# Performance work log

Measured on AMD Instinct MI355X. Metric: run time of the kernel, lower is better.

The kernel has to match this reference:

```python
import jax, jax.numpy as jnp
import numpy as np

B, T, C, H, N = 4, 4096, 1024, 16, 64
D_DECAY, D_AAA, D_MV, D_GATE = 64, 64, 32, 160
EPS_GN = 1e-5 * 8 ** 2  # GroupNorm eps = 1e-5 * head_size_divisor**2


def _k(i):
    return jax.random.fold_in(jax.random.key(0), i)


def setup_inputs():
    p = {}
    p["x"] = jax.random.normal(_k(1), (B, T, C), jnp.float32)
    p["v_first"] = jax.random.normal(_k(2), (B, T, C), jnp.float32)
    for i, name in enumerate(["x_r", "x_w", "x_k", "x_v", "x_a", "x_g"]):
        p[name] = jax.random.uniform(_k(10 + i), (1, 1, C), jnp.float32)
    p["w0"] = jnp.linspace(-7.0, -2.0, C, dtype=jnp.float32).reshape(1, 1, C) + 0.5
    p["w1"] = jax.random.normal(_k(20), (C, D_DECAY), jnp.float32) * 0.02
    p["w2"] = jax.random.normal(_k(21), (D_DECAY, C), jnp.float32) * 0.02
    p["a0"] = jax.random.normal(_k(22), (1, 1, C), jnp.float32) * 0.02
    p["a1"] = jax.random.normal(_k(23), (C, D_AAA), jnp.float32) * 0.02
    p["a2"] = jax.random.normal(_k(24), (D_AAA, C), jnp.float32) * 0.02
    p["v0"] = jnp.ones((1, 1, C), jnp.float32)
    p["v1"] = jax.random.normal(_k(25), (C, D_MV), jnp.float32) * 0.02
    p["v2"] = jax.random.normal(_k(26), (D_MV, C), jnp.float32) * 0.02
    p["g1"] = jax.random.normal(_k(27), (C, D_GATE), jnp.float32) * 0.02
    p["g2"] = jax.random.normal(_k(28), (D_GATE, C), jnp.float32) * 0.02
    p["k_k"] = jnp.full((1, 1, C), 0.85, jnp.float32)
    p["k_a"] = jnp.ones((1, 1, C), jnp.float32)
    p["r_k"] = jax.random.normal(_k(29), (H, N), jnp.float32) * 0.02
    s = 0.5 / C ** 0.5
    p["Wr"] = jax.random.uniform(_k(30), (C, C), jnp.float32, -s, s)
    p["Wk"] = jax.random.uniform(_k(31), (C, C), jnp.float32, -0.1 * s, 0.1 * s)
    p["Wv"] = jax.random.uniform(_k(32), (C, C), jnp.float32, -s, s)
    p["Wo"] = jax.random.uniform(_k(33), (C, C), jnp.float32, -s, s)
    p["ln_w"] = jnp.ones((C,), jnp.float32)
    p["ln_b"] = jnp.zeros((C,), jnp.float32)
    p["alpha"] = jnp.array(0.5, jnp.float32)
    return p


def _wkv_scan(ins, reverse):
    # ins: tuple of time-major (T,B,H,N) arrays: r, decay, k, v, a, b
    def step(S, inp):
        r_t, d_t, k_t, v_t, a_t, b_t = inp
        sa = jnp.einsum('bhij,bhj->bhi', S, a_t)  # in-context removal term
        S = (S * d_t[:, :, None, :]
             + sa[..., None] * b_t[:, :, None, :]
             + v_t[..., None] * k_t[:, :, None, :])
        return S, jnp.einsum('bhij,bhj->bhi', S, r_t)
    S0 = jnp.zeros((B, H, N, N), jnp.float32)
    return jax.lax.scan(step, S0, ins, reverse=reverse)[1]


def reference(x, v_first, x_r, x_w, x_k, x_v, x_a, x_g, w0, w1, w2, a0, a1, a2,
              v0, v1, v2, g1, g2, k_k, k_a, r_k, Wr, Wk, Wv, Wo, ln_w, ln_b, alpha):
    xx = jnp.pad(x, ((0, 0), (1, 0), (0, 0)))[:, :T, :] - x  # token shift
    xr = x + xx * x_r
    xw = x + xx * x_w
    xk = x + xx * x_k
    xv = x + xx * x_v
    xa = x + xx * x_a
    xg = x + xx * x_g
    r = xr @ Wr.T
    w = -jax.nn.softplus(-(w0 + jnp.tanh(xw @ w1) @ w2)) - 0.5
    k = xk @ Wk.T
    v = xv @ Wv.T
    v = v + (v_first - v) * jax.nn.sigmoid(v0 + (xv @ v1) @ v2)  # layer_id != 0
    a = jax.nn.sigmoid(a0 + (xa @ a1) @ a2)
    g = jax.nn.sigmoid(xg @ g1) @ g2
    kk = (k * k_k).reshape(B, T, H, N)
    kk = kk / jnp.maximum(jnp.linalg.norm(kk, axis=-1, keepdims=True), 1e-12)
    k = k * (1.0 + (a - 1.0) * k_a)
    rh = r.reshape(B, T, H, N)
    kh = k.reshape(B, T, H, N)
    vh = v.reshape(B, T, H, N)
    dec = jnp.exp(-jnp.exp(w.reshape(B, T, H, N)))  # per-channel decay
    ah = -kk
    bh = kk * a.reshape(B, T, H, N)
    tm = lambda z: jnp.transpose(z, (1, 0, 2, 3))  # -> (T,B,H,N)
    ins = (tm(rh), tm(dec), tm(kh), tm(vh), tm(ah), tm(bh))
    y_f = _wkv_scan(ins, reverse=False)
    y_b = _wkv_scan(ins, reverse=True)
    y = alpha * y_f + (1.0 - alpha) * y_b  # bidirectional blend (alpha)
    y = jnp.transpose(y, (1, 0, 2, 3))  # (B,T,H,N)
    mu = y.mean(-1, keepdims=True)
    var = y.var(-1, keepdims=True)
    y = (y - mu) / jnp.sqrt(var + EPS_GN)  # GroupNorm(H groups)
    y = y * ln_w.reshape(1, 1, H, N) + ln_b.reshape(1, 1, H, N)
    y = y + (rh * kh * r_k).sum(-1, keepdims=True) * vh
    out = (y.reshape(B, T, C) * g) @ Wo.T
    return (out, v_first)
```

## Files before the change

### kernel.cpp

```cpp
#include <hip/hip_runtime.h>
#include <hip/hip_bf16.h>
#include <math.h>

#define BB 4
#define TT 4096
#define CC 1024
#define HH 16
#define NN 64
#define BT (BB*TT)
#define EPS_GN 6.4e-4f
#define TMAX (TT-1)
#define LCH 64
#define CB 8
#define NB 8
#define STR 68

typedef __attribute__((ext_vector_type(8))) short bf16x8;
typedef __attribute__((ext_vector_type(4))) float f32x4;

__device__ __forceinline__ float sigmoidf_(float x) {
    return 1.0f / (1.0f + expf(-x));
}

__device__ __forceinline__ float waveReduceSum(float v) {
    #pragma unroll
    for (int off = 32; off > 0; off >>= 1)
        v += __shfl_xor(v, off, 64);
    return v;
}

__device__ __forceinline__ unsigned short f2bf(float f) {
    unsigned u = __float_as_uint(f);
    u += 0x7FFFu + ((u >> 16) & 1u);
    return (unsigned short)(u >> 16);
}
__device__ __forceinline__ float bf2f(unsigned short h) {
    return __uint_as_float(((unsigned)h) << 16);
}

__device__ __forceinline__ void gll16(const unsigned short* g, unsigned short* l) {
    __builtin_amdgcn_global_load_lds(
        (__attribute__((address_space(1))) void*)(g),
        (__attribute__((address_space(3))) void*)(l), 16, 0, 0);
}

template<int SA0,int SA1,int SB0,int SB1>
__device__ __forceinline__ void gemm64(const float* __restrict__ A,
                                       const float* __restrict__ B,
                                       float acc[4][4], int tr, int tc) {
    #pragma unroll 2
    for (int kx = 0; kx < 64; kx += 4) {
        float a_[4][4];
        if (SA0 == 1) {
            #pragma unroll
            for (int kk = 0; kk < 4; kk++) {
                float4 t = *(const float4*)&A[tr + (kx + kk) * SA1];
                a_[0][kk] = t.x; a_[1][kk] = t.y; a_[2][kk] = t.z; a_[3][kk] = t.w;
            }
        } else {
            #pragma unroll
            for (int r = 0; r < 4; r++) {
                float4 t = *(const float4*)&A[(tr + r) * SA0 + kx];
                a_[r][0] = t.x; a_[r][1] = t.y; a_[r][2] = t.z; a_[r][3] = t.w;
            }
        }
        float b_[4][4];
        if (SB0 == 1) {
            #pragma unroll
            for (int kk = 0; kk < 4; kk++) {
                float4 t = *(const float4*)&B[tc + (kx + kk) * SB1];
                b_[0][kk] = t.x; b_[1][kk] = t.y; b_[2][kk] = t.z; b_[3][kk] = t.w;
            }
        } else {
            #pragma unroll
            for (int cq = 0; cq < 4; cq++) {
                float4 t = *(const float4*)&B[(tc + cq) * SB0 + kx];
                b_[cq][0] = t.x; b_[cq][1] = t.y; b_[cq][2] = t.z; b_[cq][3] = t.w;
            }
        }
        #pragma unroll
        for (int r = 0; r < 4; r++)
            #pragma unroll
            for (int cq = 0; cq < 4; cq++)
                #pragma unroll
                for (int kk = 0; kk < 4; kk++)
                    acc[r][cq] = fmaf(a_[r][kk], b_[cq][kk], acc[r][cq]);
    }
}

template<bool DOMIX>
__global__ __launch_bounds__(256) void conv_split(
    const float* __restrict__ X, const float* __restrict__ mix,
    unsigned short* __restrict__ Hi, unsigned short* __restrict__ Lo,
    int ngroups)
{
    int g = blockIdx.x * 256 + threadIdx.x;
    if (g >= ngroups) return;
    int m = g >> 7;
    int k = (g & 127) * 8;
    const float* px = X + (size_t)m * CC + k;
    float a[8];
    {
        float4 x0 = *(const float4*)px;
        float4 x1 = *(const float4*)(px + 4);
        a[0]=x0.x; a[1]=x0.y; a[2]=x0.z; a[3]=x0.w;
        a[4]=x1.x; a[5]=x1.y; a[6]=x1.z; a[7]=x1.w;
    }
    if (DOMIX) {
        float4 p0, p1;
        if ((m & (TT - 1)) == 0) {
            p0 = make_float4(0.f,0.f,0.f,0.f); p1 = p0;
        } else {
            p0 = *(const float4*)(px - CC);
            p1 = *(const float4*)(px - CC + 4);
        }
        float4 m0 = *(const float4*)(mix + k);
        float4 m1 = *(const float4*)(mix + k + 4);
        float pv[8] = {p0.x,p0.y,p0.z,p0.w,p1.x,p1.y,p1.z,p1.w};
        float mv[8] = {m0.x,m0.y,m0.z,m0.w,m1.x,m1.y,m1.z,m1.w};
        #pragma unroll
        for (int j = 0; j < 8; j++) a[j] += (pv[j] - a[j]) * mv[j];
    }
    unsigned short hi[8], lo[8];
    #pragma unroll
    for (int j = 0; j < 8; j++) {
        hi[j] = f2bf(a[j]);
        lo[j] = f2bf(a[j] - bf2f(hi[j]));
    }
    uint4 H, L;
    H.x = (unsigned)hi[0] | ((unsigned)hi[1] << 16);
    H.y = (unsigned)hi[2] | ((unsigned)hi[3] << 16);
    H.z = (unsigned)hi[4] | ((unsigned)hi[5] << 16);
    H.w = (unsigned)hi[6] | ((unsigned)hi[7] << 16);
    L.x = (unsigned)lo[0] | ((unsigned)lo[1] << 16);
    L.y = (unsigned)lo[2] | ((unsigned)lo[3] << 16);
    L.z = (unsigned)lo[4] | ((unsigned)lo[5] << 16);
    L.w = (unsigned)lo[6] | ((unsigned)lo[7] << 16);
    *(uint4*)(Hi + (size_t)g * 8) = H;
    *(uint4*)(Lo + (size_t)g * 8) = L;
}

__global__ __launch_bounds__(256) void conv_split_x3(
    const float* __restrict__ X,
    const float* __restrict__ mr, const float* __restrict__ mk,
    const float* __restrict__ mv,
    unsigned short* __restrict__ rH, unsigned short* __restrict__ rL,
    unsigned short* __restrict__ kH, unsigned short* __restrict__ kL,
    unsigned short* __restrict__ vH, unsigned short* __restrict__ vL)
{
    int g = blockIdx.x * 256 + threadIdx.x;
    int m = g >> 7;
    int k = (g & 127) * 8;
    const float* px = X + (size_t)m * CC + k;
    float xv8[8], pv[8];
    {
        float4 x0 = *(const float4*)px;
        float4 x1 = *(const float4*)(px + 4);
        xv8[0]=x0.x; xv8[1]=x0.y; xv8[2]=x0.z; xv8[3]=x0.w;
        xv8[4]=x1.x; xv8[5]=x1.y; xv8[6]=x1.z; xv8[7]=x1.w;
    }
    if ((m & (TT - 1)) == 0) {
        #pragma unroll
        for (int j = 0; j < 8; j++) pv[j] = 0.f;
    } else {
        float4 p0 = *(const float4*)(px - CC);
        float4 p1 = *(const float4*)(px - CC + 4);
        pv[0]=p0.x; pv[1]=p0.y; pv[2]=p0.z; pv[3]=p0.w;
        pv[4]=p1.x; pv[5]=p1.y; pv[6]=p1.z; pv[7]=p1.w;
    }
    const float* mixes[3] = {mr, mk, mv};
    unsigned short* His[3] = {rH, kH, vH};
    unsigned short* Los[3] = {rL, kL, vL};
    #pragma unroll
    for (int s = 0; s < 3; s++) {
        float4 m0 = *(const float4*)(mixes[s] + k);
        float4 m1 = *(const float4*)(mixes[s] + k + 4);
        float mv8[8] = {m0.x,m0.y,m0.z,m0.w,m1.x,m1.y,m1.z,m1.w};
        unsigned short hi[8], lo[8];
        #pragma unroll
        for (int j = 0; j < 8; j++) {
            float a = xv8[j] + (pv[j] - xv8[j]) * mv8[j];
            hi[j] = f2bf(a);
            lo[j] = f2bf(a - bf2f(hi[j]));
        }
        uint4 H, L;
        H.x = (unsigned)hi[0] | ((unsigned)hi[1] << 16);
        H.y = (unsigned)hi[2] | ((unsigned)hi[3] << 16);
        H.z = (unsigned)hi[4] | ((unsigned)hi[5] << 16);
        H.w = (unsigned)hi[6] | ((unsigned)hi[7] << 16);
        L.x = (unsigned)lo[0] | ((unsigned)lo[1] << 16);
        L.y = (unsigned)lo[2] | ((unsigned)lo[3] << 16);
        L.z = (unsigned)lo[4] | ((unsigned)lo[5] << 16);
        L.w = (unsigned)lo[6] | ((unsigned)lo[7] << 16);
        *(uint4*)(His[s] + (size_t)g * 8) = H;
        *(uint4*)(Los[s] + (size_t)g * 8) = L;
    }
}

__global__ __launch_bounds__(256) void conv_w2(
    const float* __restrict__ W, int K, int Kp,
    unsigned short* __restrict__ Hi, unsigned short* __restrict__ Lo)
{
    int idx = blockIdx.x * 256 + threadIdx.x;
    int nk8 = Kp >> 3;
    if (idx >= CC * nk8) return;
    int n = idx / nk8, k0 = (idx - n * nk8) * 8;
    unsigned short h8[8], l8[8];
    #pragma unroll
    for (int j = 0; j < 8; j++) {
        int k = k0 + j;
        float v = (k < K) ? W[(size_t)k * CC + n] : 0.f;
        h8[j] = f2bf(v);
        l8[j] = f2bf(v - bf2f(h8[j]));
    }
    uint4 H, L;
    H.x = (unsigned)h8[0] | ((unsigned)h8[1] << 16);
    H.y = (unsigned)h8[2] | ((unsigned)h8[3] << 16);
    H.z = (unsigned)h8[4] | ((unsigned)h8[5] << 16);
    H.w = (unsigned)h8[6] | ((unsigned)h8[7] << 16);
    L.x = (unsigned)l8[0] | ((unsigned)l8[1] << 16);
    L.y = (unsigned)l8[2] | ((unsigned)l8[3] << 16);
    L.z = (unsigned)l8[4] | ((unsigned)l8[5] << 16);
    L.w = (unsigned)l8[6] | ((unsigned)l8[7] << 16);
    *(uint4*)(Hi + (size_t)n * Kp + k0) = H;
    *(uint4*)(Lo + (size_t)n * Kp + k0) = L;
}

__global__ __launch_bounds__(256, 2) void gemm_split_bf16(
    const unsigned short* __restrict__ Ah, const unsigned short* __restrict__ Al,
    const unsigned short* __restrict__ Bh, const unsigned short* __restrict__ Bl,
    float* __restrict__ Out)
{
    __shared__ __align__(16) unsigned short lds[4][128 * 64];
    const int tid = threadIdx.x;
    const int lane = tid & 63;
    const int wave = tid >> 6;
    const int wm = (wave >> 1) * 64, wn = (wave & 1) * 64;
    const int wg = blockIdx.x;
    const int xcd = wg & 7;
    const int j = wg >> 3;
    const int m0 = ((j >> 3) * 8 + xcd) * 128;
    const int n0 = (j & 7) * 128;

    f32x4 acc[4][4];
    #pragma unroll
    for (int i = 0; i < 4; i++)
        #pragma unroll
        for (int jj = 0; jj < 4; jj++)
            acc[i][jj] = (f32x4){0.f, 0.f, 0.f, 0.f};

    for (int k0 = 0; k0 < CC; k0 += 64) {
        #pragma unroll
        for (int p = 0; p < 4; p++) {
            const unsigned short* sbase = (p == 0) ? Ah : (p == 1) ? Al
                                        : (p == 2) ? Bh : Bl;
            const int rbase = (p < 2) ? m0 : n0;
            #pragma unroll
            for (int i = 0; i < 4; i++) {
                int slot = i * 256 + wave * 64 + lane;
                int row = slot >> 3, gsl = slot & 7;
                const unsigned short* src = sbase
                    + (size_t)(rbase + row) * CC + k0 + ((gsl ^ (row & 7)) * 8);
                gll16(src, &lds[p][(size_t)(i * 256 + wave * 64) * 8]);
            }
        }
        __syncthreads();

        #pragma unroll
        for (int ks = 0; ks < 2; ks++) {
            bf16x8 bhf[4], blf[4];
            #pragma unroll
            for (int nt = 0; nt < 4; nt++) {
                int col = wn + nt * 16 + (lane & 15);
                int gk = ks * 4 + (lane >> 4);
                int el = col * 64 + ((gk ^ (col & 7)) * 8);
                bhf[nt] = *(const bf16x8*)&lds[2][el];
                blf[nt] = *(const bf16x8*)&lds[3][el];
            }
            #pragma unroll
            for (int mt = 0; mt < 4; mt++) {
                int row = wm + mt * 16 + (lane & 15);
                int gk = ks * 4 + (lane >> 4);
                int el = row * 64 + ((gk ^ (row & 7)) * 8);
                bf16x8 ahf = *(const bf16x8*)&lds[0][el];
                bf16x8 alf = *(const bf16x8*)&lds[1][el];
                #pragma unroll
                for (int nt = 0; nt < 4; nt++) {
                    acc[mt][nt] = __builtin_amdgcn_mfma_f32_16x16x32_bf16(
                        ahf, bhf[nt], acc[mt][nt], 0, 0, 0);
                    acc[mt][nt] = __builtin_amdgcn_mfma_f32_16x16x32_bf16(
                        alf, bhf[nt], acc[mt][nt], 0, 0, 0);
                    acc[mt][nt] = __builtin_amdgcn_mfma_f32_16x16x32_bf16(
                        ahf, blf[nt], acc[mt][nt], 0, 0, 0);
                }
            }
        }
        __syncthreads();
    }
    float* cf = (float*)&lds[0][0];
    #pragma unroll
    for (int pass = 0; pass < 2; ++pass) {
        __syncthreads();
        if ((wave >> 1) == pass) {
            #pragma unroll
            for (int mt = 0; mt < 4; mt++)
                #pragma unroll
                for (int nt = 0; nt < 4; nt++)
                    #pragma unroll
                    for (int r = 0; r < 4; r++) {
                        int row = mt * 16 + (lane >> 4) * 4 + r;
                        int col = wn + nt * 16 + (lane & 15);
                        cf[row * 132 + col] = acc[mt][nt][r];
                    }
        }
        __syncthreads();
        #pragma unroll
        for (int i = 0; i < 8; i++) {
            int g = tid + 256 * i;
            int row = g >> 5, c4 = (g & 31) * 4;
            float4 v = *(float4*)&cf[row * 132 + c4];
            *(float4*)&Out[(size_t)(m0 + pass * 64 + row) * CC + n0 + c4] = v;
        }
    }
}

__global__ __launch_bounds__(256) void lora1_all(
    const float* __restrict__ X,
    const float* __restrict__ w1, const float* __restrict__ a1,
    const float* __restrict__ v1, const float* __restrict__ g1,
    const float* __restrict__ xw, const float* __restrict__ xa,
    const float* __restrict__ xv, const float* __restrict__ xg,
    unsigned short* __restrict__ awh, unsigned short* __restrict__ awl,
    unsigned short* __restrict__ aah, unsigned short* __restrict__ aal,
    unsigned short* __restrict__ avh, unsigned short* __restrict__ avl,
    unsigned short* __restrict__ agh, unsigned short* __restrict__ agl)
{
    const int y = blockIdx.y;
    const float* W; const float* mix; unsigned short *Hi, *Lo;
    int Ncols, n0, epi, Kp;
    if (y == 0)      { W=w1; mix=xw; Hi=awh; Lo=awl; Ncols=64;  n0=0;          epi=1; Kp=64;  }
    else if (y == 1) { W=a1; mix=xa; Hi=aah; Lo=aal; Ncols=64;  n0=0;          epi=0; Kp=64;  }
    else if (y == 2) { W=v1; mix=xv; Hi=avh; Lo=avl; Ncols=32;  n0=0;          epi=0; Kp=64;  }
    else             { W=g1; mix=xg; Hi=agh; Lo=agl; Ncols=160; n0=(y-3)*64;   epi=2; Kp=192; }

    __shared__ float As[8][64];
    __shared__ float Bs[8][64];
    const int tid = threadIdx.x;
    const int m0 = blockIdx.x * 64;
    const int sr  = tid >> 1;
    const int skq = (tid & 1) * 4;
    const int t2  = tid - 128;
    const int bkr = t2 >> 4;
    const int bnq = (t2 & 15) * 4;
    const int tm = (tid >> 3) * 2;
    const int tn = (tid & 7) * 8;

    float acc[2][8];
    #pragma unroll
    for (int i = 0; i < 2; i++)
        #pragma unroll
        for (int j = 0; j < 8; j++) acc[i][j] = 0.f;

    auto ldAm = [&](int gm, int gk) -> float4 {
        const float* px = X + (size_t)gm * CC + gk;
        float4 xvv = *(const float4*)px;
        float4 pv;
        if ((gm & (TT - 1)) == 0) pv = make_float4(0.f, 0.f, 0.f, 0.f);
        else pv = *(const float4*)(px - CC);
        float4 mv = *(const float4*)(mix + gk);
        xvv.x += (pv.x - xvv.x) * mv.x;
        xvv.y += (pv.y - xvv.y) * mv.y;
        xvv.z += (pv.z - xvv.z) * mv.z;
        xvv.w += (pv.w - xvv.w) * mv.w;
        return xvv;
    };

    float4 aR = make_float4(0.f, 0.f, 0.f, 0.f);
    float4 bR = make_float4(0.f, 0.f, 0.f, 0.f);
    if (tid < 128) {
        aR = ldAm(m0 + sr, skq);
    } else {
        int gn = n0 + bnq;
        bR = (gn < Ncols) ? *(const float4*)(W + (size_t)bkr * Ncols + gn)
                          : make_float4(0.f, 0.f, 0.f, 0.f);
    }

    for (int k0 = 0; k0 < CC; k0 += 8) {
        __syncthreads();
        if (tid < 128) {
            As[skq + 0][sr] = aR.x;
            As[skq + 1][sr] = aR.y;
            As[skq + 2][sr] = aR.z;
            As[skq + 3][sr] = aR.w;
        } else {
            *(float4*)&Bs[bkr][bnq] = bR;
        }
        __syncthreads();

        if (k0 + 8 < CC) {
            if (tid < 128) {
                aR = ldAm(m0 + sr, k0 + 8 + skq);
            } else {
                int gn = n0 + bnq;
                bR = (gn < Ncols) ? *(const float4*)(W + (size_t)(k0 + 8 + bkr) * Ncols + gn)
                                  : make_float4(0.f, 0.f, 0.f, 0.f);
            }
        }

        #pragma unroll
        for (int kk = 0; kk < 8; ++kk) {
            float av[2], bv[8];
            av[0] = As[kk][tm];
            av[1] = As[kk][tm + 1];
            *(float4*)&bv[0] = *(const float4*)&Bs[kk][tn];
            *(float4*)&bv[4] = *(const float4*)&Bs[kk][tn + 4];
            #pragma unroll
            for (int i = 0; i < 2; i++)
                #pragma unroll
                for (int j = 0; j < 8; j++)
                    acc[i][j] = fmaf(av[i], bv[j], acc[i][j]);
        }
    }

    #pragma unroll
    for (int i = 0; i < 2; i++) {
        int gm = m0 + tm + i;
        int gn = n0 + tn;
        if (gn < Kp) {
            unsigned short h8[8], l8[8];
            #pragma unroll
            for (int j = 0; j < 8; j++) {
                float v = 0.f;
                if (gn + j < Ncols) {
                    v = acc[i][j];
                    if (epi == 1) v = tanhf(v);
                    else if (epi == 2) v = sigmoidf_(v);
                }
                h8[j] = f2bf(v);
                l8[j] = f2bf(v - bf2f(h8[j]));
            }
            uint4 H, L;
            H.x = (unsigned)h8[0] | ((unsigned)h8[1] << 16);
            H.y = (unsigned)h8[2] | ((unsigned)h8[3] << 16);
            H.z = (unsigned)h8[4] | ((unsigned)h8[5] << 16);
            H.w = (unsigned)h8[6] | ((unsigned)h8[7] << 16);
            L.x = (unsigned)l8[0] | ((unsigned)l8[1] << 16);
            L.y = (unsigned)l8[2] | ((unsigned)l8[3] << 16);
            L.z = (unsigned)l8[4] | ((unsigned)l8[5] << 16);
            L.w = (unsigned)l8[6] | ((unsigned)l8[7] << 16);
            *(uint4*)(Hi + (size_t)gm * Kp + gn) = H;
            *(uint4*)(Lo + (size_t)gm * Kp + gn) = L;
        }
    }
}

__global__ __launch_bounds__(256, 3) void lora2_mfma(
    const unsigned short* __restrict__ awh, const unsigned short* __restrict__ awl,
    const unsigned short* __restrict__ aah, const unsigned short* __restrict__ aal,
    const unsigned short* __restrict__ avh, const unsigned short* __restrict__ avl,
    const unsigned short* __restrict__ agh, const unsigned short* __restrict__ agl,
    const unsigned short* __restrict__ w2h, const unsigned short* __restrict__ w2l,
    const unsigned short* __restrict__ a2h, const unsigned short* __restrict__ a2l,
    const unsigned short* __restrict__ v2h, const unsigned short* __restrict__ v2l,
    const unsigned short* __restrict__ g2h, const unsigned short* __restrict__ g2l,
    const float* __restrict__ w0, const float* __restrict__ a0v,
    const float* __restrict__ v0v, const float* __restrict__ v_first,
    float* __restrict__ decb, float* __restrict__ ab,
    float* __restrict__ vbuf, float* __restrict__ gb)
{
    __shared__ __align__(16) unsigned short lds[24576];
    const int z = blockIdx.z;
    const unsigned short *Ah, *Al, *Bh, *Bl; int Kp;
    if (z == 0)      { Ah = awh; Al = awl; Bh = w2h; Bl = w2l; Kp = 64;  }
    else if (z == 1) { Ah = aah; Al = aal; Bh = a2h; Bl = a2l; Kp = 64;  }
    else if (z == 2) { Ah = avh; Al = avl; Bh = v2h; Bl = v2l; Kp = 64;  }
    else             { Ah = agh; Al = agl; Bh = g2h; Bl = g2l; Kp = 192; }

    const int tid = threadIdx.x, lane = tid & 63, wave = tid >> 6;
    const int wm = (wave >> 1) * 64, wn = (wave & 1) * 32;
    const int m0 = blockIdx.x * 128, n0 = blockIdx.y * 64;

    f32x4 acc[4][2];
    #pragma unroll
    for (int i = 0; i < 4; i++)
        #pragma unroll
        for (int jj = 0; jj < 2; jj++)
            acc[i][jj] = (f32x4){0.f, 0.f, 0.f, 0.f};

    for (int k0 = 0; k0 < Kp; k0 += 64) {
        #pragma unroll
        for (int p = 0; p < 2; p++) {
            const unsigned short* sbase = (p == 0) ? Ah : Al;
            #pragma unroll
            for (int i = 0; i < 4; i++) {
                int slot = i * 256 + wave * 64 + lane;
                int row = slot >> 3, gsl = slot & 7;
                const unsigned short* src = sbase
                    + (size_t)(m0 + row) * Kp + k0 + ((gsl ^ (row & 7)) * 8);
                gll16(src, &lds[(size_t)(p * 8192) + (size_t)(i * 256 + wave * 64) * 8]);
            }
        }
        #pragma unroll
        for (int p = 0; p < 2; p++) {
            const unsigned short* sbase = (p == 0) ? Bh : Bl;
            #pragma unroll
            for (int i = 0; i < 2; i++) {
                int slot = i * 256 + wave * 64 + lane;
                int row = slot >> 3, gsl = slot & 7;
                const unsigned short* src = sbase
                    + (size_t)(n0 + row) * Kp + k0 + ((gsl ^ (row & 7)) * 8);
                gll16(src, &lds[(size_t)(16384 + p * 4096) + (size_t)(i * 256 + wave * 64) * 8]);
            }
        }
        __syncthreads();

        #pragma unroll
        for (int ks = 0; ks < 2; ks++) {
            bf16x8 bhf[2], blf[2];
            #pragma unroll
            for (int nt = 0; nt < 2; nt++) {
                int col = wn + nt * 16 + (lane & 15);
                int gk = ks * 4 + (lane >> 4);
                int el = col * 64 + ((gk ^ (col & 7)) * 8);
                bhf[nt] = *(const bf16x8*)&lds[16384 + el];
                blf[nt] = *(const bf16x8*)&lds[20480 + el];
            }
            #pragma unroll
            for (int mt = 0; mt < 4; mt++) {
                int row = wm + mt * 16 + (lane & 15);
                int gk = ks * 4 + (lane >> 4);
                int el = row * 64 + ((gk ^ (row & 7)) * 8);
                bf16x8 ahf = *(const bf16x8*)&lds[el];
                bf16x8 alf = *(const bf16x8*)&lds[8192 + el];
                #pragma unroll
                for (int nt = 0; nt < 2; nt++) {
                    acc[mt][nt] = __builtin_amdgcn_mfma_f32_16x16x32_bf16(
                        ahf, bhf[nt], acc[mt][nt], 0, 0, 0);
                    acc[mt][nt] = __builtin_amdgcn_mfma_f32_16x16x32_bf16(
                        alf, bhf[nt], acc[mt][nt], 0, 0, 0);
                    acc[mt][nt] = __builtin_amdgcn_mfma_f32_16x16x32_bf16(
                        ahf, blf[nt], acc[mt][nt], 0, 0, 0);
                }
            }
        }
        __syncthreads();
    }
    float* cf = (float*)&lds[0];
    #pragma unroll
    for (int mt = 0; mt < 4; mt++)
        #pragma unroll
        for (int nt = 0; nt < 2; nt++)
            #pragma unroll
            for (int r = 0; r < 4; r++) {
                int row = wm + mt * 16 + (lane >> 4) * 4 + r;
                int col = wn + nt * 16 + (lane & 15);
                cf[row * 68 + col] = acc[mt][nt][r];
            }
    __syncthreads();
    #pragma unroll
    for (int i = 0; i < 8; i++) {
        int idx = tid + 256 * i;
        int row = idx >> 4, c4 = (idx & 15) * 4;
        float4 v = *(float4*)&cf[row * 68 + c4];
        int gm = m0 + row;
        int c = n0 + c4;
        size_t off = (size_t)gm * CC + c;
        if (z == 0) {
            float4 w0q = *(const float4*)(w0 + c);
            float4 o;
            o.x = expf(-expf(-log1pf(expf(-(w0q.x + v.x))) - 0.5f));
            o.y = expf(-expf(-log1pf(expf(-(w0q.y + v.y))) - 0.5f));
            o.z = expf(-expf(-log1pf(expf(-(w0q.z + v.z))) - 0.5f));
            o.w = expf(-expf(-log1pf(expf(-(w0q.w + v.w))) - 0.5f));
            *(float4*)&decb[off] = o;
        } else if (z == 1) {
            float4 a0q = *(const float4*)(a0v + c);
            float4 o;
            o.x = sigmoidf_(a0q.x + v.x);
            o.y = sigmoidf_(a0q.y + v.y);
            o.z = sigmoidf_(a0q.z + v.z);
            o.w = sigmoidf_(a0q.w + v.w);
            *(float4*)&ab[off] = o;
        } else if (z == 2) {
            float4 v0q = *(const float4*)(v0v + c);
            float4 vr = *(const float4*)&vbuf[off];
            float4 vf = *(const float4*)&v_first[off];
            float4 o;
            o.x = vr.x + (vf.x - vr.x) * sigmoidf_(v0q.x + v.x);
            o.y = vr.y + (vf.y - vr.y) * sigmoidf_(v0q.y + v.y);
            o.z = vr.z + (vf.z - vr.z) * sigmoidf_(v0q.z + v.z);
            o.w = vr.w + (vf.w - vr.w) * sigmoidf_(v0q.w + v.w);
            *(float4*)&vbuf[off] = o;
        } else {
            *(float4*)&gb[off] = v;
        }
    }
}

__global__ __launch_bounds__(256) void wkvA(
    const float* __restrict__ kb, const float* __restrict__ ab,
    const float* __restrict__ vb, const float* __restrict__ decb,
    const float* __restrict__ k_k, const float* __restrict__ k_a,
    float* __restrict__ Gb, float* __restrict__ Ub,
    float* __restrict__ Bpb, float* __restrict__ Kpb,
    float* __restrict__ wcb, int cb)
{
    __shared__ __align__(16) float sAp[64 * STR];
    __shared__ __align__(16) float sBp[64 * STR];
    __shared__ __align__(16) float sKp[64 * STR];
    __shared__ __align__(16) float sT [64 * STR];
    __shared__ float sSeg[4][64];
    const int inst = blockIdx.x;
    const int bhd = inst >> 3, lc = inst & 7;
    const int dir = bhd & 1, bh = bhd >> 1, b = bh >> 4, h = bh & 15;
    const int c64 = (cb * CB + lc) * LCH;
    const int tid = threadIdx.x;
    const int lane = tid & 63, seg = tid >> 6;
    const int ch = h * 64 + lane;
    const size_t gbase = (size_t)inst * 4096;

    float loc[16];
    {
        float run = 1.f;
        #pragma unroll
        for (int i = 0; i < 16; i++) {
            int p = seg * 16 + i;
            int t = dir ? (TMAX - (c64 + p)) : (c64 + p);
            float d = decb[((size_t)(b * TT + t)) * CC + ch];
            run *= d; loc[i] = run;
        }
        sSeg[seg][lane] = run;
    }
    __syncthreads();
    float pre = 1.f;
    for (int s2 = 0; s2 < seg; ++s2) pre *= sSeg[s2][lane];
    {
        const float kkl = k_k[ch], kal = k_a[ch];
        #pragma unroll
        for (int i = 0; i < 16; i++) {
            int p = seg * 16 + i;
            int t = dir ? (TMAX - (c64 + p)) : (c64 + p);
            size_t ra = ((size_t)(b * TT + t)) * CC + ch;
            float kraw = kb[ra], asig = ab[ra];
            float kkv = kraw * kkl;
            float s2 = waveReduceSum(kkv * kkv);
            float kkn = kkv / fmaxf(sqrtf(s2), 1e-12f);
            float wc = loc[i] * pre;
            float wx = (i == 0) ? pre : loc[i - 1] * pre;
            float apv = -kkn * wx;
            float bpv = kkn * asig / wc;
            float kpv = kraw * (1.f + (asig - 1.f) * kal) / wc;
            sAp[lane * STR + p] = apv;
            sBp[lane * STR + p] = bpv;
            sKp[lane * STR + p] = kpv;
            Bpb[gbase + p * 64 + lane] = bpv;
            Kpb[gbase + p * 64 + lane] = kpv;
            wcb[gbase + p * 64 + lane] = wc;
        }
    }
    __syncthreads();

    const int tr = (tid >> 4) * 4, tc = (tid & 15) * 4;
    {
        float acc[4][4] = {};
        gemm64<1, STR, 1, STR>(sAp, sKp, acc, tr, tc);
        #pragma unroll
        for (int r = 0; r < 4; r++)
            #pragma unroll
            for (int cq = 0; cq < 4; cq++)
                sT[(tr + r) * STR + tc + cq] = (tc + cq < tr + r) ? acc[r][cq] : 0.f;
    }
    __syncthreads();
    {
        float accY[4][4] = {};
        const float* vbase = vb + ((size_t)(b * TT + (dir ? (TMAX - c64) : c64))) * CC
                           + h * 64 + tc;
        const ptrdiff_t vstep = dir ? -(ptrdiff_t)CC : (ptrdiff_t)CC;
        #pragma unroll 2
        for (int j4 = 0; j4 < 64; j4 += 4) {
            float a_[4][4];
            #pragma unroll
            for (int r = 0; r < 4; r++) {
                float4 t4 = *(const float4*)&sT[(tr + r) * STR + j4];
                a_[r][0] = t4.x; a_[r][1] = t4.y; a_[r][2] = t4.z; a_[r][3] = t4.w;
            }
            float4 vq[4];
            #pragma unroll
            for (int kk = 0; kk < 4; kk++)
                vq[kk] = *(const float4*)(vbase + (ptrdiff_t)(j4 + kk) * vstep);
            #pragma unroll
            for (int r = 0; r < 4; r++) {
                accY[r][0] = fmaf(a_[r][0], vq[0].x, fmaf(a_[r][1], vq[1].x,
                             fmaf(a_[r][2], vq[2].x, fmaf(a_[r][3], vq[3].x, accY[r][0]))));
                accY[r][1] = fmaf(a_[r][0], vq[0].y, fmaf(a_[r][1], vq[1].y,
                             fmaf(a_[r][2], vq[2].y, fmaf(a_[r][3], vq[3].y, accY[r][1]))));
                accY[r][2] = fmaf(a_[r][0], vq[0].z, fmaf(a_[r][1], vq[1].z,
                             fmaf(a_[r][2], vq[2].z, fmaf(a_[r][3], vq[3].z, accY[r][2]))));
                accY[r][3] = fmaf(a_[r][0], vq[0].w, fmaf(a_[r][1], vq[1].w,
                             fmaf(a_[r][2], vq[2].w, fmaf(a_[r][3], vq[3].w, accY[r][3]))));
            }
        }
        #pragma unroll
        for (int r = 0; r < 4; r++)
            #pragma unroll
            for (int cq = 0; cq < 4; cq++)
                sKp[(tr + r) * STR + tc + cq] = accY[r][cq];
    }
    __syncthreads();
    {
        float acc[4][4] = {};
        gemm64<1, STR, 1, STR>(sAp, sBp, acc, tr, tc);
        #pragma unroll
        for (int r = 0; r < 4; r++)
            #pragma unroll
            for (int cq = 0; cq < 4; cq++)
                sT[(tr + r) * STR + tc + cq] = (tc + cq < tr + r) ? acc[r][cq] : 0.f;
    }
    __syncthreads();
    if (tid < 64) {
        for (int r = 0; r < 64; ++r) {
            float acc = 0.f;
            for (int s = 0; s < r; ++s)
                acc = fmaf(sT[r * STR + s], sBp[s * STR + tid], acc);
            sBp[r * STR + tid] = (r == tid) ? 1.f : acc;
        }
    }
    __syncthreads();
    {
        float accG[4][4] = {};
        gemm64<STR, 1, STR, 1>(sBp, sAp, accG, tr, tc);
        float accU[4][4] = {};
        gemm64<STR, 1, 1, STR>(sBp, sKp, accU, tr, tc);
        #pragma unroll
        for (int r = 0; r < 4; r++) {
            *(float4*)&Gb[gbase + (tr + r) * 64 + tc] =
                make_float4(accG[r][0], accG[r][1], accG[r][2], accG[r][3]);
            *(float4*)&Ub[gbase + (tr + r) * 64 + tc] =
                make_float4(accU[r][0], accU[r][1], accU[r][2], accU[r][3]);
        }
    }
}

__global__ __launch_bounds__(256) void wkvB(
    const float* __restrict__ vb,
    const float* __restrict__ Gb, float* __restrict__ Ub,
    const float* __restrict__ Bpb, const float* __restrict__ Kpb,
    const float* __restrict__ wcb, float* __restrict__ S0b,
    float* __restrict__ Scur, int cb)
{
    __shared__ __align__(16) float sS[64 * STR];
    __shared__ __align__(16) float sG[64 * STR];
    __shared__ __align__(16) float sU[64 * STR];
    __shared__ __align__(16) float sB[64 * STR];
    __shared__ __align__(16) float sK[64 * STR];
    __shared__ __align__(16) float sV[64 * STR];
    const int bhd = blockIdx.x;
    const int dir = bhd & 1, bh = bhd >> 1, b = bh >> 4, h = bh & 15;
    const int tid = threadIdx.x;
    const int tr = (tid >> 4) * 4, tc = (tid & 15) * 4;

    for (int i = tid; i < 4096; i += 256)
        sS[(i >> 6) * STR + (i & 63)] = Scur[(size_t)bhd * 4096 + i];
    __syncthreads();

    for (int lc = 0; lc < CB; ++lc) {
        const int inst = bhd * CB + lc;
        const size_t gbase = (size_t)inst * 4096;
        const int c64 = (cb * CB + lc) * LCH;
        for (int i = tid; i < 4096; i += 256) {
            int rr = i >> 6, jj = i & 63;
            sG[rr * STR + jj] = Gb[gbase + i];
            sB[rr * STR + jj] = Bpb[gbase + i];
            sK[rr * STR + jj] = Kpb[gbase + i];
            int t = dir ? (TMAX - (c64 + rr)) : (c64 + rr);
            sV[rr * STR + jj] = vb[((size_t)(b * TT + t)) * CC + h * 64 + jj];
            S0b[gbase + i] = sS[rr * STR + jj];
        }
        __syncthreads();
        {
            float acc[4][4];
            #pragma unroll
            for (int r = 0; r < 4; r++) {
                float4 u0 = *(const float4*)&Ub[gbase + (tr + r) * 64 + tc];
                acc[r][0] = u0.x; acc[r][1] = u0.y; acc[r][2] = u0.z; acc[r][3] = u0.w;
            }
            gemm64<STR, 1, STR, 1>(sG, sS, acc, tr, tc);
            #pragma unroll
            for (int r = 0; r < 4; r++) {
                #pragma unroll
                for (int cq = 0; cq < 4; cq++) sU[(tr + r) * STR + tc + cq] = acc[r][cq];
                *(float4*)&Ub[gbase + (tr + r) * 64 + tc] =
                    make_float4(acc[r][0], acc[r][1], acc[r][2], acc[r][3]);
            }
        }
        __syncthreads();
        {
            float acc[4][4] = {};
            gemm64<1, STR, 1, STR>(sU, sB, acc, tr, tc);
            gemm64<1, STR, 1, STR>(sV, sK, acc, tr, tc);
            float w63[4];
            #pragma unroll
            for (int cq = 0; cq < 4; cq++) w63[cq] = wcb[gbase + 63 * 64 + tc + cq];
            #pragma unroll
            for (int r = 0; r < 4; r++)
                #pragma unroll
                for (int cq = 0; cq < 4; cq++) {
                    float sv = sS[(tr + r) * STR + tc + cq];
                    acc[r][cq] = (sv + acc[r][cq]) * w63[cq];
                }
            #pragma unroll
            for (int r = 0; r < 4; r++)
                #pragma unroll
                for (int cq = 0; cq < 4; cq++)
                    sS[(tr + r) * STR + tc + cq] = acc[r][cq];
        }
        __syncthreads();
    }
    for (int i = tid; i < 4096; i += 256)
        Scur[(size_t)bhd * 4096 + i] = sS[(i >> 6) * STR + (i & 63)];
}

__global__ __launch_bounds__(256) void wkvC(
    const float* __restrict__ rb, const float* __restrict__ vb,
    const float* __restrict__ Bpb, const float* __restrict__ Kpb,
    const float* __restrict__ Ub, const float* __restrict__ S0b,
    const float* __restrict__ wcb, const float* __restrict__ alpha_p,
    float* __restrict__ yb, int cb)
{
    __shared__ __align__(16) float sR[64 * STR];
    __shared__ __align__(16) float sO[64 * STR];
    __shared__ __align__(16) float sT2[64 * STR];
    const int inst = blockIdx.x;
    const int bhd = inst >> 3, lc = inst & 7;
    const int dir = bhd & 1, bh = bhd >> 1, b = bh >> 4, h = bh & 15;
    const int c64 = (cb * CB + lc) * LCH;
    const int tid = threadIdx.x, lane = tid & 63, seg = tid >> 6;
    const size_t gbase = (size_t)inst * 4096;
    const float alpha = alpha_p[0];
    const float wscale = dir ? (1.f - alpha) : alpha;
    const bool first = (cb < NB / 2);

    #pragma unroll
    for (int i = 0; i < 16; i++) {
        int p = seg * 16 + i;
        int t = dir ? (TMAX - (c64 + p)) : (c64 + p);
        size_t ra = ((size_t)(b * TT + t)) * CC + h * 64 + lane;
        float wc = wcb[gbase + p * 64 + lane];
        sR[lane * STR + p] = rb[ra] * wc;
        sO[lane * STR + p] = Bpb[gbase + p * 64 + lane];
    }
    __syncthreads();
    const int tr = (tid >> 4) * 4, tc = (tid & 15) * 4;
    float accO[4][4] = {};
    {
        float acc[4][4] = {};
        gemm64<1, STR, 1, STR>(sR, sO, acc, tr, tc);
        #pragma unroll
        for (int r = 0; r < 4; r++)
            #pragma unroll
            for (int cq = 0; cq < 4; cq++)
                sT2[(tr + r) * STR + tc + cq] = (tc + cq <= tr + r) ? acc[r][cq] : 0.f;
    }
    __syncthreads();
    for (int i = tid; i < 4096; i += 256)
        sO[(i >> 6) * STR + (i & 63)] = Ub[gbase + i];
    __syncthreads();
    gemm64<STR, 1, 1, STR>(sT2, sO, accO, tr, tc);
    __syncthreads();
    #pragma unroll
    for (int i = 0; i < 16; i++) {
        int p = seg * 16 + i;
        sO[lane * STR + p] = Kpb[gbase + p * 64 + lane];
    }
    __syncthreads();
    {
        float acc[4][4] = {};
        gemm64<1, STR, 1, STR>(sR, sO, acc, tr, tc);
        #pragma unroll
        for (int r = 0; r < 4; r++)
            #pragma unroll
            for (int cq = 0; cq < 4; cq++)
                sT2[(tr + r) * STR + tc + cq] = (tc + cq <= tr + r) ? acc[r][cq] : 0.f;
    }
    __syncthreads();
    #pragma unroll
    for (int i = 0; i < 16; i++) {
        int p = seg * 16 + i;
        int t = dir ? (TMAX - (c64 + p)) : (c64 + p);
        sO[p * STR + lane] = vb[((size_t)(b * TT + t)) * CC + h * 64 + lane];
    }
    __syncthreads();
    gemm64<STR, 1, 1, STR>(sT2, sO, accO, tr, tc);
    __syncthreads();
    for (int i = tid; i < 4096; i += 256)
        sO[(i >> 6) * STR + (i & 63)] = S0b[gbase + i];
    __syncthreads();
    gemm64<1, STR, STR, 1>(sR, sO, accO, tr, tc);
    #pragma unroll
    for (int r = 0; r < 4; r++) {
        int p = tr + r;
        int t = dir ? (TMAX - (c64 + p)) : (c64 + p);
        float* yp = &yb[((size_t)(b * TT + t)) * CC + h * 64 + tc];
        float4 o;
        if (first) {
            o.x = wscale * accO[r][0];
            o.y = wscale * accO[r][1];
            o.z = wscale * accO[r][2];
            o.w = wscale * accO[r][3];
        } else {
            float4 old = *(float4*)yp;
            o.x = old.x + wscale * accO[r][0];
            o.y = old.y + wscale * accO[r][1];
            o.z = old.z + wscale * accO[r][2];
            o.w = old.w + wscale * accO[r][3];
        }
        *(float4*)yp = o;
    }
}

__global__ __launch_bounds__(256) void post_kernel(
    const float* __restrict__ yb, const float* __restrict__ rbv,
    const float* __restrict__ kbv, const float* __restrict__ abv,
    const float* __restrict__ vbv, const float* __restrict__ gbv,
    const float* __restrict__ kaw, const float* __restrict__ r_k,
    const float* __restrict__ ln_w, const float* __restrict__ ln_b,
    unsigned short* __restrict__ zh, unsigned short* __restrict__ zl)
{
    const int t = blockIdx.x;
    const int tid = threadIdx.x;
    const size_t base = (size_t)t * CC;
    #pragma unroll
    for (int j = 0; j < 4; j++) {
        int c = tid + 256 * j;
        float y = yb[base + c];
        float s1 = waveReduceSum(y);
        float s2 = waveReduceSum(y * y);
        float mu = s1 * (1.0f / 64.0f);
        float var = s2 * (1.0f / 64.0f) - mu * mu;
        float yn = (y - mu) * rsqrtf(var + EPS_GN);
        yn = yn * ln_w[c] + ln_b[c];
        float rv = rbv[base + c];
        float kf = kbv[base + c] * (1.0f + (abv[base + c] - 1.0f) * kaw[c]);
        float vv = vbv[base + c];
        float dot = waveReduceSum(rv * kf * r_k[c]);
        yn += dot * vv;
        float z = yn * gbv[base + c];
        unsigned short h = f2bf(z);
        zh[base + c] = h;
        zl[base + c] = f2bf(z - bf2f(h));
    }
}

extern "C" void kernel_launch(void* const* d_in, const int* in_sizes, int n_in,
                              void* d_out, int out_size, void* d_ws, size_t ws_size,
                              hipStream_t stream)
{
    (void)in_sizes; (void)n_in; (void)out_size; (void)ws_size;
    const float* x      = (const float*)d_in[0];
    const float* vfirst = (const float*)d_in[1];
    const float* x_r    = (const float*)d_in[2];
    const float* x_w    = (const float*)d_in[3];
    const float* x_k    = (const float*)d_in[4];
    const float* x_v    = (const float*)d_in[5];
    const float* x_a    = (const float*)d_in[6];
    const float* x_g    = (const float*)d_in[7];
    const float* w0     = (const float*)d_in[8];
    const float* w1     = (const float*)d_in[9];
    const float* w2     = (const float*)d_in[10];
    const float* a0     = (const float*)d_in[11];
    const float* a1     = (const float*)d_in[12];
    const float* a2     = (const float*)d_in[13];
    const float* v0     = (const float*)d_in[14];
    const float* v1     = (const float*)d_in[15];
    const float* v2     = (const float*)d_in[16];
    const float* g1     = (const float*)d_in[17];
    const float* g2     = (const float*)d_in[18];
    const float* k_k    = (const float*)d_in[19];
    const float* k_a    = (const float*)d_in[20];
    const float* r_k    = (const float*)d_in[21];
    const float* Wr     = (const float*)d_in[22];
    const float* Wk     = (const float*)d_in[23];
    const float* Wv     = (const float*)d_in[24];
    const float* Wo     = (const float*)d_in[25];
    const float* ln_w   = (const float*)d_in[26];
    const float* ln_b   = (const float*)d_in[27];
    const float* alpha  = (const float*)d_in[28];

    const size_t SZ = (size_t)BT * CC;
    const size_t CHB = (size_t)1024 * 4096;
    float* ws   = (float*)d_ws;
    float* rb   = ws + 0 * SZ;
    float* kb   = ws + 1 * SZ;
    float* vb   = ws + 2 * SZ;
    float* decb = ws + 3 * SZ;
    float* ab   = ws + 4 * SZ;
    float* actf = ws + 5 * SZ;
    unsigned short* awh = (unsigned short*)actf;
    unsigned short* awl = awh + (size_t)BT * 64;
    unsigned short* aah = awl + (size_t)BT * 64;
    unsigned short* aal = aah + (size_t)BT * 64;
    unsigned short* avh = aal + (size_t)BT * 64;
    unsigned short* avl = avh + (size_t)BT * 64;
    unsigned short* agh = avl + (size_t)BT * 64;
    unsigned short* agl = agh + (size_t)BT * 192;
    float* Gb   = actf + (size_t)BT * 384;
    float* Ub   = Gb + CHB;
    float* Bpb  = Ub + CHB;
    float* Kpb  = Bpb + CHB;
    float* S0b  = Kpb + CHB;
    float* wcb  = S0b + CHB;
    float* Scur = wcb + CHB;
    unsigned short* Whb = (unsigned short*)(Scur + (size_t)128 * 4096);
    unsigned short* Wlb = Whb + (size_t)CC * CC;
    unsigned short* w2th = Wlb + (size_t)CC * CC;
    unsigned short* w2tl = w2th + (size_t)CC * 64;
    unsigned short* a2th = w2tl + (size_t)CC * 64;
    unsigned short* a2tl = a2th + (size_t)CC * 64;
    unsigned short* v2th = a2tl + (size_t)CC * 64;
    unsigned short* v2tl = v2th + (size_t)CC * 64;
    unsigned short* g2th = v2tl + (size_t)CC * 64;
    unsigned short* g2tl = g2th + (size_t)CC * 192;
    float* outp = (float*)d_out;
    unsigned short* xrh = (unsigned short*)outp;
    unsigned short* xrl = xrh + SZ;
    unsigned short* xkh = xrl + SZ;
    unsigned short* xkl = xkh + SZ;
    unsigned short* xvh = (unsigned short*)decb;
    unsigned short* xvl = xvh + SZ;
    float* gb   = outp;
    float* yb   = outp + SZ;
    unsigned short* zAh = (unsigned short*)decb;
    unsigned short* zAl = zAh + SZ;

    dim3 blk(256);
    const int NG_A = BT * (CC / 8);
    const int NG_W = CC * (CC / 8);
    dim3 gridA(NG_A / 256), gridW(NG_W / 256);
    dim3 gridG(1024);

    conv_split_x3<<<gridA, blk, 0, stream>>>(x, x_r, x_k, x_v,
                                             xrh, xrl, xkh, xkl, xvh, xvl);
    conv_split<false><<<gridW, blk, 0, stream>>>(Wr, nullptr, Whb, Wlb, NG_W);
    gemm_split_bf16<<<gridG, blk, 0, stream>>>(xrh, xrl, Whb, Wlb, rb);
    conv_split<false><<<gridW, blk, 0, stream>>>(Wk, nullptr, Whb, Wlb, NG_W);
    gemm_split_bf16<<<gridG, blk, 0, stream>>>(xkh, xkl, Whb, Wlb, kb);
    conv_split<false><<<gridW, blk, 0, stream>>>(Wv, nullptr, Whb, Wlb, NG_W);
    gemm_split_bf16<<<gridG, blk, 0, stream>>>(xvh, xvl, Whb, Wlb, vb);

    conv_w2<<<dim3(32), blk, 0, stream>>>(w2, 64, 64, w2th, w2tl);
    conv_w2<<<dim3(32), blk, 0, stream>>>(a2, 64, 64, a2th, a2tl);
    conv_w2<<<dim3(32), blk, 0, stream>>>(v2, 32, 64, v2th, v2tl);
    conv_w2<<<dim3(96), blk, 0, stream>>>(g2, 160, 192, g2th, g2tl);

    lora1_all<<<dim3(BT / 64, 6), blk, 0, stream>>>(x, w1, a1, v1, g1,
        x_w, x_a, x_v, x_g, awh, awl, aah, aal, avh, avl, agh, agl);
    lora2_mfma<<<dim3(BT / 128, CC / 64, 4), blk, 0, stream>>>(
        awh, awl, aah, aal, avh, avl, agh, agl,
        w2th, w2tl, a2th, a2tl, v2th, v2tl, g2th, g2tl,
        w0, a0, v0, vfirst, decb, ab, vb, gb);

    hipMemsetAsync(Scur, 0, (size_t)128 * 4096 * sizeof(float), stream);
    for (int cb = 0; cb < NB; ++cb) {
        wkvA<<<dim3(1024), blk, 0, stream>>>(kb, ab, vb, decb, k_k, k_a,
                                             Gb, Ub, Bpb, Kpb, wcb, cb);
        wkvB<<<dim3(128), blk, 0, stream>>>(vb, Gb, Ub, Bpb, Kpb, wcb, S0b, Scur, cb);
        wkvC<<<dim3(1024), blk, 0, stream>>>(rb, vb, Bpb, Kpb, Ub, S0b, wcb,
                                             alpha, yb, cb);
    }

    post_kernel<<<dim3(BT), blk, 0, stream>>>(yb, rb, kb, ab, vb, gb, k_a, r_k,
                                              ln_w, ln_b, zAh, zAl);
    conv_split<false><<<gridW, blk, 0, stream>>>(Wo, nullptr, Whb, Wlb, NG_W);
    hipMemcpyAsync(outp + SZ, vfirst, SZ * sizeof(float),
                   hipMemcpyDeviceToDevice, stream);
    gemm_split_bf16<<<gridG, blk, 0, stream>>>(zAh, zAl, Whb, Wlb, outp);
}
```

Before: 3.118 ms.

## Batch weight conversion and r/k/v GEMMs; halve GEMM K-tile, drop LDS epilogue

All four projection weights are converted to hi/lo bf16 in one launch into a 4-slot buffer. The r, k and v projections now run as a single GEMM launch with a grid y-dimension selecting inputs and outputs, removing the serial per-weight conversion and GEMM launches. The GEMM K-step is halved to 32 so LDS use drops and launch bounds allow 3 blocks per CU. The LDS-staged coalesced output store is replaced by direct per-lane scalar stores, which may write to global memory less efficiently.

After: 3.139 ms. About the same (+0.7%).

```diff
diff --git a/kernel.cpp b/kernel.cpp
--- a/kernel.cpp
+++ b/kernel.cpp
@@ -86,58 +86,6 @@
                 for (int kk = 0; kk < 4; kk++)
                     acc[r][cq] = fmaf(a_[r][kk], b_[cq][kk], acc[r][cq]);
     }
-}
-
-template<bool DOMIX>
-__global__ __launch_bounds__(256) void conv_split(
-    const float* __restrict__ X, const float* __restrict__ mix,
-    unsigned short* __restrict__ Hi, unsigned short* __restrict__ Lo,
-    int ngroups)
-{
-    int g = blockIdx.x * 256 + threadIdx.x;
-    if (g >= ngroups) return;
-    int m = g >> 7;
-    int k = (g & 127) * 8;
-    const float* px = X + (size_t)m * CC + k;
-    float a[8];
-    {
-        float4 x0 = *(const float4*)px;
-        float4 x1 = *(const float4*)(px + 4);
-        a[0]=x0.x; a[1]=x0.y; a[2]=x0.z; a[3]=x0.w;
-        a[4]=x1.x; a[5]=x1.y; a[6]=x1.z; a[7]=x1.w;
-    }
-    if (DOMIX) {
-        float4 p0, p1;
-        if ((m & (TT - 1)) == 0) {
-            p0 = make_float4(0.f,0.f,0.f,0.f); p1 = p0;
-        } else {
-            p0 = *(const float4*)(px - CC);
-            p1 = *(const float4*)(px - CC + 4);
-        }
-        float4 m0 = *(const float4*)(mix + k);
-        float4 m1 = *(const float4*)(mix + k + 4);
-        float pv[8] = {p0.x,p0.y,p0.z,p0.w,p1.x,p1.y,p1.z,p1.w};
-        float mv[8] = {m0.x,m0.y,m0.z,m0.w,m1.x,m1.y,m1.z,m1.w};
-        #pragma unroll
-        for (int j = 0; j < 8; j++) a[j] += (pv[j] - a[j]) * mv[j];
-    }
-    unsigned short hi[8], lo[8];
-    #pragma unroll
-    for (int j = 0; j < 8; j++) {
-        hi[j] = f2bf(a[j]);
-        lo[j] = f2bf(a[j] - bf2f(hi[j]));
-    }
-    uint4 H, L;
-    H.x = (unsigned)hi[0] | ((unsigned)hi[1] << 16);
-    H.y = (unsigned)hi[2] | ((unsigned)hi[3] << 16);
-    H.z = (unsigned)hi[4] | ((unsigned)hi[5] << 16);
-    H.w = (unsigned)hi[6] | ((unsigned)hi[7] << 16);
-    L.x = (unsigned)lo[0] | ((unsigned)lo[1] << 16);
-    L.y = (unsigned)lo[2] | ((unsigned)lo[3] << 16);
-    L.z = (unsigned)lo[4] | ((unsigned)lo[5] << 16);
-    L.w = (unsigned)lo[6] | ((unsigned)lo[7] << 16);
-    *(uint4*)(Hi + (size_t)g * 8) = H;
-    *(uint4*)(Lo + (size_t)g * 8) = L;
 }
 
 __global__ __launch_bounds__(256) void conv_split_x3(
@@ -197,6 +145,45 @@
     }
 }
 
+
+__global__ __launch_bounds__(256) void conv_w4(
+    const float* __restrict__ Wr, const float* __restrict__ Wk,
+    const float* __restrict__ Wv, const float* __restrict__ Wo,
+    unsigned short* __restrict__ Hi, unsigned short* __restrict__ Lo)
+{
+    int g = blockIdx.x * 256 + threadIdx.x;
+    int y = blockIdx.y;
+    const float* W = (y == 0) ? Wr : (y == 1) ? Wk : (y == 2) ? Wv : Wo;
+    size_t doff = (size_t)y * CC * CC;
+    int m = g >> 7;
+    int k = (g & 127) * 8;
+    const float* px = W + (size_t)m * CC + k;
+    float a[8];
+    {
+        float4 x0 = *(const float4*)px;
+        float4 x1 = *(const float4*)(px + 4);
+        a[0]=x0.x; a[1]=x0.y; a[2]=x0.z; a[3]=x0.w;
+        a[4]=x1.x; a[5]=x1.y; a[6]=x1.z; a[7]=x1.w;
+    }
+    unsigned short hi[8], lo[8];
+    #pragma unroll
+    for (int j = 0; j < 8; j++) {
+        hi[j] = f2bf(a[j]);
+        lo[j] = f2bf(a[j] - bf2f(hi[j]));
+    }
+    uint4 H, L;
+    H.x = (unsigned)hi[0] | ((unsigned)hi[1] << 16);
+    H.y = (unsigned)hi[2] | ((unsigned)hi[3] << 16);
+    H.z = (unsigned)hi[4] | ((unsigned)hi[5] << 16);
+    H.w = (unsigned)hi[6] | ((unsigned)hi[7] << 16);
+    L.x = (unsigned)lo[0] | ((unsigned)lo[1] << 16);
+    L.y = (unsigned)lo[2] | ((unsigned)lo[3] << 16);
+    L.z = (unsigned)lo[4] | ((unsigned)lo[5] << 16);
+    L.w = (unsigned)lo[6] | ((unsigned)lo[7] << 16);
+    *(uint4*)(Hi + doff + (size_t)g * 8) = H;
+    *(uint4*)(Lo + doff + (size_t)g * 8) = L;
+}
+
 __global__ __launch_bounds__(256) void conv_w2(
     const float* __restrict__ W, int K, int Kp,
     unsigned short* __restrict__ Hi, unsigned short* __restrict__ Lo)
@@ -226,15 +213,22 @@
     *(uint4*)(Lo + (size_t)n * Kp + k0) = L;
 }
 
-__global__ __launch_bounds__(256, 2) void gemm_split_bf16(
-    const unsigned short* __restrict__ Ah, const unsigned short* __restrict__ Al,
-    const unsigned short* __restrict__ Bh, const unsigned short* __restrict__ Bl,
-    float* __restrict__ Out)
+__global__ __launch_bounds__(256, 3) void gemm_split_bf16(
+    const unsigned short* __restrict__ A0h, const unsigned short* __restrict__ A0l,
+    const unsigned short* __restrict__ A1h, const unsigned short* __restrict__ A1l,
+    const unsigned short* __restrict__ A2h, const unsigned short* __restrict__ A2l,
+    const unsigned short* __restrict__ W4h, const unsigned short* __restrict__ W4l,
+    float* __restrict__ O0, float* __restrict__ O1, float* __restrict__ O2,
+    int wbase)
 {
-    __shared__ __align__(16) unsigned short lds[4][128 * 64];
-    const int tid = threadIdx.x;
-    const int lane = tid & 63;
-    const int wave = tid >> 6;
+    __shared__ __align__(16) unsigned short lds[4][128 * 32];
+    const int sel = blockIdx.y;
+    const unsigned short* Ah = (sel == 0) ? A0h : (sel == 1) ? A1h : A2h;
+    const unsigned short* Al = (sel == 0) ? A0l : (sel == 1) ? A1l : A2l;
+    float* Out = (sel == 0) ? O0 : (sel == 1) ? O1 : O2;
+    const unsigned short* Bh = W4h + (size_t)(wbase + sel) * CC * CC;
+    const unsigned short* Bl = W4l + (size_t)(wbase + sel) * CC * CC;
+    const int tid = threadIdx.x, lane = tid & 63, wave = tid >> 6;
     const int wm = (wave >> 1) * 64, wn = (wave & 1) * 64;
     const int wg = blockIdx.x;
     const int xcd = wg & 7;
@@ -249,79 +243,61 @@
         for (int jj = 0; jj < 4; jj++)
             acc[i][jj] = (f32x4){0.f, 0.f, 0.f, 0.f};
 
-    for (int k0 = 0; k0 < CC; k0 += 64) {
+    for (int k0 = 0; k0 < CC; k0 += 32) {
         #pragma unroll
         for (int p = 0; p < 4; p++) {
             const unsigned short* sbase = (p == 0) ? Ah : (p == 1) ? Al
                                         : (p == 2) ? Bh : Bl;
             const int rbase = (p < 2) ? m0 : n0;
             #pragma unroll
-            for (int i = 0; i < 4; i++) {
+            for (int i = 0; i < 2; i++) {
                 int slot = i * 256 + wave * 64 + lane;
-                int row = slot >> 3, gsl = slot & 7;
+                int row = slot >> 2, gsl = slot & 3;
                 const unsigned short* src = sbase
-                    + (size_t)(rbase + row) * CC + k0 + ((gsl ^ (row & 7)) * 8);
+                    + (size_t)(rbase + row) * CC + k0 + ((gsl ^ (row & 3)) * 8);
                 gll16(src, &lds[p][(size_t)(i * 256 + wave * 64) * 8]);
             }
         }
         __syncthreads();
 
-        #pragma unroll
-        for (int ks = 0; ks < 2; ks++) {
-            bf16x8 bhf[4], blf[4];
+        const int gk = lane >> 4;
+        bf16x8 bhf[4], blf[4];
+        #pragma unroll
+        for (int nt = 0; nt < 4; nt++) {
+            int col = wn + nt * 16 + (lane & 15);
+            int el = col * 32 + ((gk ^ (col & 3)) * 8);
+            bhf[nt] = *(const bf16x8*)&lds[2][el];
+            blf[nt] = *(const bf16x8*)&lds[3][el];
+        }
+        #pragma unroll
+        for (int mt = 0; mt < 4; mt++) {
+            int row = wm + mt * 16 + (lane & 15);
+            int el = row * 32 + ((gk ^ (row & 3)) * 8);
+            bf16x8 ahf = *(const bf16x8*)&lds[0][el];
+            bf16x8 alf = *(const bf16x8*)&lds[1][el];
             #pragma unroll
             for (int nt = 0; nt < 4; nt++) {
-                int col = wn + nt * 16 + (lane & 15);
-                int gk = ks * 4 + (lane >> 4);
-                int el = col * 64 + ((gk ^ (col & 7)) * 8);
-                bhf[nt] = *(const bf16x8*)&lds[2][el];
-                blf[nt] = *(const bf16x8*)&lds[3][el];
-            }
-            #pragma unroll
-            for (int mt = 0; mt < 4; mt++) {
-                int row = wm + mt * 16 + (lane & 15);
-                int gk = ks * 4 + (lane >> 4);
-                int el = row * 64 + ((gk ^ (row & 7)) * 8);
-                bf16x8 ahf = *(const bf16x8*)&lds[0][el];
-                bf16x8 alf = *(const bf16x8*)&lds[1][el];
-                #pragma unroll
-                for (int nt = 0; nt < 4; nt++) {
-                    acc[mt][nt] = __builtin_amdgcn_mfma_f32_16x16x32_bf16(
-                        ahf, bhf[nt], acc[mt][nt], 0, 0, 0);
-                    acc[mt][nt] = __builtin_amdgcn_mfma_f32_16x16x32_bf16(
-                        alf, bhf[nt], acc[mt][nt], 0, 0, 0);
-                    acc[mt][nt] = __builtin_amdgcn_mfma_f32_16x16x32_bf16(
-                        ahf, blf[nt], acc[mt][nt], 0, 0, 0);
-                }
+                acc[mt][nt] = __builtin_amdgcn_mfma_f32_16x16x32_bf16(
+                    ahf, bhf[nt], acc[mt][nt], 0, 0, 0);
+                acc[mt][nt] = __builtin_amdgcn_mfma_f32_16x16x32_bf16(
+                    alf, bhf[nt], acc[mt][nt], 0, 0, 0);
+                acc[mt][nt] = __builtin_amdgcn_mfma_f32_16x16x32_bf16(
+                    ahf, blf[nt], acc[mt][nt], 0, 0, 0);
             }
         }
         __syncthreads();
     }
-    float* cf = (float*)&lds[0][0];
-    #pragma unroll
-    for (int pass = 0; pass < 2; ++pass) {
-        __syncthreads();
-        if ((wave >> 1) == pass) {
-            #pragma unroll
-            for (int mt = 0; mt < 4; mt++)
-                #pragma unroll
-                for (int nt = 0; nt < 4; nt++)
-                    #pragma unroll
-                    for (int r = 0; r < 4; r++) {
-                        int row = mt * 16 + (lane >> 4) * 4 + r;
-                        int col = wn + nt * 16 + (lane & 15);
-                        cf[row * 132 + col] = acc[mt][nt][r];
-                    }
-        }
-        __syncthreads();
-        #pragma unroll
-        for (int i = 0; i < 8; i++) {
-            int g = tid + 256 * i;
-            int row = g >> 5, c4 = (g & 31) * 4;
-            float4 v = *(float4*)&cf[row * 132 + c4];
-            *(float4*)&Out[(size_t)(m0 + pass * 64 + row) * CC + n0 + c4] = v;
-        }
-    }
+    #pragma unroll
+    for (int mt = 0; mt < 4; mt++)
+        #pragma unroll
+        for (int nt = 0; nt < 4; nt++) {
+            int col = n0 + wn + nt * 16 + (lane & 15);
+            #pragma unroll
+            for (int r = 0; r < 4; r++) {
+                int row = m0 + wm + mt * 16 + (lane >> 4) * 4 + r;
+                Out[(size_t)row * CC + col] = acc[mt][nt][r];
+            }
+        }
 }
 
 __global__ __launch_bounds__(256) void lora1_all(
@@ -1010,9 +986,9 @@
     float* S0b  = Kpb + CHB;
     float* wcb  = S0b + CHB;
     float* Scur = wcb + CHB;
-    unsigned short* Whb = (unsigned short*)(Scur + (size_t)128 * 4096);
-    unsigned short* Wlb = Whb + (size_t)CC * CC;
-    unsigned short* w2th = Wlb + (size_t)CC * CC;
+    unsigned short* W4h = (unsigned short*)(Scur + (size_t)128 * 4096);
+    unsigned short* W4l = W4h + (size_t)CC * CC * 4;
+    unsigned short* w2th = W4l + (size_t)CC * CC * 4;
     unsigned short* w2tl = w2th + (size_t)CC * 64;
     unsigned short* a2th = w2tl + (size_t)CC * 64;
     unsigned short* a2tl = a2th + (size_t)CC * 64;
@@ -1034,18 +1010,13 @@
 
     dim3 blk(256);
     const int NG_A = BT * (CC / 8);
-    const int NG_W = CC * (CC / 8);
-    dim3 gridA(NG_A / 256), gridW(NG_W / 256);
-    dim3 gridG(1024);
+    dim3 gridA(NG_A / 256);
 
     conv_split_x3<<<gridA, blk, 0, stream>>>(x, x_r, x_k, x_v,
                                              xrh, xrl, xkh, xkl, xvh, xvl);
-    conv_split<false><<<gridW, blk, 0, stream>>>(Wr, nullptr, Whb, Wlb, NG_W);
-    gemm_split_bf16<<<gridG, blk, 0, stream>>>(xrh, xrl, Whb, Wlb, rb);
-    conv_split<false><<<gridW, blk, 0, stream>>>(Wk, nullptr, Whb, Wlb, NG_W);
-    gemm_split_bf16<<<gridG, blk, 0, stream>>>(xkh, xkl, Whb, Wlb, kb);
-    conv_split<false><<<gridW, blk, 0, stream>>>(Wv, nullptr, Whb, Wlb, NG_W);
-    gemm_split_bf16<<<gridG, blk, 0, stream>>>(xvh, xvl, Whb, Wlb, vb);
+    conv_w4<<<dim3(512, 4), blk, 0, stream>>>(Wr, Wk, Wv, Wo, W4h, W4l);
+    gemm_split_bf16<<<dim3(1024, 3), blk, 0, stream>>>(
+        xrh, xrl, xkh, xkl, xvh, xvl, W4h, W4l, rb, kb, vb, 0);
 
     conv_w2<<<dim3(32), blk, 0, stream>>>(w2, 64, 64, w2th, w2tl);
     conv_w2<<<dim3(32), blk, 0, stream>>>(a2, 64, 64, a2th, a2tl);
@@ -1070,8 +1041,8 @@
 
     post_kernel<<<dim3(BT), blk, 0, stream>>>(yb, rb, kb, ab, vb, gb, k_a, r_k,
                                               ln_w, ln_b, zAh, zAl);
-    conv_split<false><<<gridW, blk, 0, stream>>>(Wo, nullptr, Whb, Wlb, NG_W);
     hipMemcpyAsync(outp + SZ, vfirst, SZ * sizeof(float),
                    hipMemcpyDeviceToDevice, stream);
-    gemm_split_bf16<<<gridG, blk, 0, stream>>>(zAh, zAl, Whb, Wlb, outp);
-}
+    gemm_split_bf16<<<dim3(1024, 1), blk, 0, stream>>>(
+        zAh, zAl, zAh, zAl, zAh, zAl, W4h, W4l, outp, outp, outp, 3);
+}
```
